# Performance work log

Measured on AMD Instinct MI355X. Metric: run time of the kernel, lower is better.

The kernel has to match this reference:

```python
import jax, jax.numpy as jnp
import numpy as np

N, K, D = 16384, 200, 64  # n_samples, n_components, n_features (8x8 patches)
LOG_2PI = np.float32(np.log(2.0 * np.pi))


def setup_inputs() -> dict:
    rng = np.random.default_rng(0)
    # Build SPD covariances and derive precisions_cholesky exactly like the module:
    # cov_chol = cholesky(cov, lower); prec_chol = solve(cov_chol, I).T
    A = rng.normal(size=(K, D, D))
    cov = A @ A.transpose(0, 2, 1) + D * np.eye(D)  # well-conditioned SPD
    cov_chol = np.linalg.cholesky(cov)  # lower triangular [K,D,D]
    eye = np.broadcast_to(np.eye(D), (K, D, D))
    prec_chol = np.linalg.solve(cov_chol, eye).transpose(0, 2, 1).astype(np.float32)
    means = rng.normal(size=(K, D)).astype(np.float32)
    key = jax.random.key(0)
    x = jax.random.normal(key, (N, D), dtype=jnp.float32)
    return {"x": x, "means": jnp.asarray(means), "prec_chol": jnp.asarray(prec_chol)}


def reference(x, means, prec_chol):
    """Batched GMM log-prob (fused version of estimate_log_prob_torch).

    log_prob[n,k] = -0.5*(D*log(2pi) + ||x_n L_k - mu_k L_k||^2) + log|det L_k|
    where L_k = precisions_cholesky[k].
    """
    n_features = x.shape[1]
    # y[n,k,e] = x @ L_k  -- one batched GEMM instead of K small matmuls
    y = jnp.einsum('nd,kde->nke', x, prec_chol)
    mu_prec = jnp.einsum('kd,kde->ke', means, prec_chol)  # mu_k @ L_k, [K,D]
    log_prob = jnp.sum(jnp.square(y - mu_prec[None, :, :]), axis=-1)  # [N,K]
    # log det of cholesky of precision = sum of log of diagonal entries
    log_det = jnp.sum(jnp.log(jnp.diagonal(prec_chol, axis1=1, axis2=2)), axis=1)  # [K]
    return -0.5 * (n_features * LOG_2PI + log_prob) + log_det[None, :]
```

## Files before the change

### kernel.cpp

```cpp
#include <hip/hip_runtime.h>
#include <hip/hip_bf16.h>
#include <stdint.h>

typedef __bf16 bf16x8 __attribute__((ext_vector_type(8)));
typedef float  f32x4  __attribute__((ext_vector_type(4)));

#define KC 200
#define KB 8
#define CBASE (-58.8120661251f)


__global__ __launch_bounds__(256) void prep_b(const float* __restrict__ prec,
                                              const float* __restrict__ means,
                                              __bf16* __restrict__ Lt,
                                              float* __restrict__ muL,
                                              float* __restrict__ ckh) {
    __shared__ float sP[64][40];
    __shared__ float sM[64];
    const int k = blockIdx.x >> 1, h = blockIdx.x & 1, tid = threadIdx.x;
    const float* pk = prec + (size_t)k * 4096 + h * 32;
    #pragma unroll
    for (int it = 0; it < 2; ++it) {
        int f4 = tid + it * 256;
        int d = f4 >> 3, c = (f4 & 7) * 4;
        float4 v = *(const float4*)(pk + (size_t)d * 64 + c);
        *(float4*)&sP[d][c] = v;
    }
    if (tid < 16) *(float4*)&sM[tid * 4] = ((const float4*)(means + (size_t)k * 64))[tid];
    __syncthreads();
    {
        int e = tid >> 3, d0 = (tid & 7) * 8;
        bf16x8 o;
        #pragma unroll
        for (int i = 0; i < 8; ++i) o[i] = (__bf16)sP[d0 + i][e];
        *(bf16x8*)(Lt + (size_t)k * 4096 + (size_t)(h * 32 + e) * 64 + d0) = o;
    }
    if (tid < 32) {
        int e = tid;
        float m = 0.f;
        #pragma unroll 8
        for (int d = 0; d < 64; ++d) m = fmaf(sM[d], sP[d][e], m);
        muL[k * 64 + h * 32 + e] = m;
        float l = __logf(sP[h * 32 + e][e]);
        #pragma unroll
        for (int mm = 16; mm >= 1; mm >>= 1) l += __shfl_xor(l, mm, 64);
        if (e == 0) ckh[h * KC + k] = l;
    }
}

#define GLL16(gp_, lp_) \
    __builtin_amdgcn_global_load_lds((__attribute__((address_space(1))) const void*)(gp_), \
                                     (__attribute__((address_space(3))) void*)(lp_), 16, 0, 0)

__global__ __launch_bounds__(256, 4) void gmm_main(const float* __restrict__ x,
                                                   const __bf16* __restrict__ Lt,
                                                   const float* __restrict__ muL,
                                                   const float* __restrict__ ckh,
                                                   float* __restrict__ out) {
    __shared__ __align__(16) __bf16 sB[2 * 4096];
    __shared__ __align__(16) float  sOut[256][12];
    __shared__ __align__(16) float  sMu[KB * 64];
    __shared__ float sCk[KB];

    const int tid  = threadIdx.x;
    const int wave = tid >> 6, lane = tid & 63;
    const int li   = lane & 15, q = lane >> 4;
    const int r8   = lane >> 3, s8 = lane & 7;
    const int row0 = blockIdx.x * 256;
    const int rowW = row0 + wave * 64;
    const int k0   = blockIdx.y * KB;
    char* sBc = (char*)sB;

    {
        const __bf16* L0 = Lt + (size_t)k0 * 4096;
        #pragma unroll
        for (int i = 0; i < 2; ++i) {
            int t = wave * 2 + i;
            GLL16(L0 + (size_t)(t * 8 + r8) * 64 + (s8 ^ r8) * 8, sBc + t * 1024);
        }
    }
    if (tid < 128) *(f32x4*)(sMu + tid * 4) = *(const f32x4*)(muL + (size_t)k0 * 64 + tid * 4);
    if (tid < KB)  sCk[tid] = ckh[k0 + tid] + ckh[KC + k0 + tid] + CBASE;

    bf16x8 af[4][2];
    #pragma unroll
    for (int tB = 0; tB < 4; ++tB) {
        const float* xr = x + (size_t)(rowW + 16 * tB + li) * 64 + q * 8;
        #pragma unroll
        for (int ks = 0; ks < 2; ++ks) {
            float4 v0 = *(const float4*)(xr + ks * 32);
            float4 v1 = *(const float4*)(xr + ks * 32 + 4);
            bf16x8 a;
            a[0] = (__bf16)v0.x; a[1] = (__bf16)v0.y; a[2] = (__bf16)v0.z; a[3] = (__bf16)v0.w;
            a[4] = (__bf16)v1.x; a[5] = (__bf16)v1.y; a[6] = (__bf16)v1.z; a[7] = (__bf16)v1.w;
            af[tB][ks] = a;
        }
    }

    #pragma unroll
    for (int kk = 0; kk < KB; ++kk) {
        __syncthreads();
        if (kk + 1 < KB) {
            const __bf16* Ln = Lt + (size_t)(k0 + kk + 1) * 4096;
            char* dst = sBc + ((kk & 1) ^ 1) * 8192;
            #pragma unroll
            for (int i = 0; i < 2; ++i) {
                int t = wave * 2 + i;
                GLL16(Ln + (size_t)(t * 8 + r8) * 64 + (s8 ^ r8) * 8, dst + t * 1024);
            }
        }
        const char* buf = sBc + (kk & 1) * 8192;
        float p[4] = {0.f, 0.f, 0.f, 0.f};

        #pragma unroll
        for (int h = 0; h < 2; ++h) {
            bf16x8 lf[2][2];
            #pragma unroll
            for (int t = 0; t < 2; ++t) {
                int e = 16 * (2 * h + t) + li;
                #pragma unroll
                for (int ks = 0; ks < 2; ++ks)
                    lf[t][ks] = *(const bf16x8*)(buf + e * 128 + (((ks * 4 + q) ^ (li & 7)) << 4));
            }
            f32x4 acc[2][4];
            #pragma unroll
            for (int t = 0; t < 2; ++t) {
                f32x4 mneg = -*(const f32x4*)(sMu + kk * 64 + 16 * (2 * h + t) + 4 * q);
                #pragma unroll
                for (int tB = 0; tB < 4; ++tB) {
                    acc[t][tB] = __builtin_amdgcn_mfma_f32_16x16x32_bf16(
                        lf[t][0], af[tB][0], mneg, 0, 0, 0);
                    acc[t][tB] = __builtin_amdgcn_mfma_f32_16x16x32_bf16(
                        lf[t][1], af[tB][1], acc[t][tB], 0, 0, 0);
                }
            }
            #pragma unroll
            for (int tB = 0; tB < 4; ++tB)
                #pragma unroll
                for (int t = 0; t < 2; ++t)
                    #pragma unroll
                    for (int r = 0; r < 4; ++r)
                        p[tB] = fmaf(acc[t][tB][r], acc[t][tB][r], p[tB]);
        }
        #pragma unroll
        for (int tB = 0; tB < 4; ++tB) {
            p[tB] += __shfl_xor(p[tB], 16, 64);
            p[tB] += __shfl_xor(p[tB], 32, 64);
        }
        float val = (q == 0) ? p[0] : (q == 1) ? p[1] : (q == 2) ? p[2] : p[3];
        sOut[wave * 64 + lane][kk] = fmaf(-0.5f, val, sCk[kk]);
    }
    __syncthreads();

    {
        f32x4 a = *(const f32x4*)&sOut[tid][0];
        f32x4 b = *(const f32x4*)&sOut[tid][4];
        float* op = out + (size_t)(row0 + tid) * KC + k0;
        *(f32x4*)op = a;
        *(f32x4*)(op + 4) = b;
    }
}

extern "C" void kernel_launch(void* const* d_in, const int* in_sizes, int n_in,
                              void* d_out, int out_size, void* d_ws, size_t ws_size,
                              hipStream_t stream) {
    const float* x     = (const float*)d_in[0];
    const float* means = (const float*)d_in[1];
    const float* prec  = (const float*)d_in[2];
    float* out = (float*)d_out;

    __bf16* Lt  = (__bf16*)d_ws;
    float*  muL = (float*)((char*)d_ws + 1638400);
    float*  ckh = (float*)((char*)d_ws + 1689600);

    prep_b<<<400, 256, 0, stream>>>(prec, means, Lt, muL, ckh);
    gmm_main<<<dim3(64, KC / KB), 256, 0, stream>>>(x, Lt, muL, ckh, out);
}
```

Before: 97.41 us.

## Double rows per block to reuse each staged precision tile across more samples

Each block now handles 512 rows instead of 256, with each wave holding 128 rows of x in registers. Every LDS-staged component matrix fragment is therefore reused across twice as many MFMAs, and half as many blocks reload the Lt tiles. The output staging buffer is transposed to a [KB][512] layout to avoid strided LDS writes, and launch bounds drop to 3 waves per SIMD to fit the larger register footprint. The costs are fewer blocks (800), which means less parallelism, and lower occupancy.

```diff
diff --git a/kernel.cpp b/kernel.cpp
--- a/kernel.cpp
+++ b/kernel.cpp
@@ -52,13 +52,13 @@
     __builtin_amdgcn_global_load_lds((__attribute__((address_space(1))) const void*)(gp_), \
                                      (__attribute__((address_space(3))) void*)(lp_), 16, 0, 0)
 
-__global__ __launch_bounds__(256, 4) void gmm_main(const float* __restrict__ x,
+__global__ __launch_bounds__(256, 3) void gmm_main(const float* __restrict__ x,
                                                    const __bf16* __restrict__ Lt,
                                                    const float* __restrict__ muL,
                                                    const float* __restrict__ ckh,
                                                    float* __restrict__ out) {
     __shared__ __align__(16) __bf16 sB[2 * 4096];
-    __shared__ __align__(16) float  sOut[256][12];
+    __shared__ __align__(16) float  sOutT[KB][512];
     __shared__ __align__(16) float  sMu[KB * 64];
     __shared__ float sCk[KB];
 
@@ -66,8 +66,8 @@
     const int wave = tid >> 6, lane = tid & 63;
     const int li   = lane & 15, q = lane >> 4;
     const int r8   = lane >> 3, s8 = lane & 7;
-    const int row0 = blockIdx.x * 256;
-    const int rowW = row0 + wave * 64;
+    const int row0 = blockIdx.x * 512;
+    const int rowW = row0 + wave * 128;
     const int k0   = blockIdx.y * KB;
     char* sBc = (char*)sB;
 
@@ -82,9 +82,9 @@
     if (tid < 128) *(f32x4*)(sMu + tid * 4) = *(const f32x4*)(muL + (size_t)k0 * 64 + tid * 4);
     if (tid < KB)  sCk[tid] = ckh[k0 + tid] + ckh[KC + k0 + tid] + CBASE;
 
-    bf16x8 af[4][2];
+    bf16x8 af[8][2];
     #pragma unroll
-    for (int tB = 0; tB < 4; ++tB) {
+    for (int tB = 0; tB < 8; ++tB) {
         const float* xr = x + (size_t)(rowW + 16 * tB + li) * 64 + q * 8;
         #pragma unroll
         for (int ks = 0; ks < 2; ++ks) {
@@ -110,52 +110,53 @@
             }
         }
         const char* buf = sBc + (kk & 1) * 8192;
-        float p[4] = {0.f, 0.f, 0.f, 0.f};
+        float p[8] = {0.f, 0.f, 0.f, 0.f, 0.f, 0.f, 0.f, 0.f};
 
         #pragma unroll
         for (int h = 0; h < 2; ++h) {
-            bf16x8 lf[2][2];
             #pragma unroll
             for (int t = 0; t < 2; ++t) {
-                int e = 16 * (2 * h + t) + li;
+                const int e = 16 * (2 * h + t) + li;
+                bf16x8 lf0 = *(const bf16x8*)(buf + e * 128 + (((0 * 4 + q) ^ (li & 7)) << 4));
+                bf16x8 lf1 = *(const bf16x8*)(buf + e * 128 + (((1 * 4 + q) ^ (li & 7)) << 4));
+                f32x4 mneg = -*(const f32x4*)(sMu + kk * 64 + 16 * (2 * h + t) + 4 * q);
+                f32x4 acc[8];
                 #pragma unroll
-                for (int ks = 0; ks < 2; ++ks)
-                    lf[t][ks] = *(const bf16x8*)(buf + e * 128 + (((ks * 4 + q) ^ (li & 7)) << 4));
-            }
-            f32x4 acc[2][4];
-            #pragma unroll
-            for (int t = 0; t < 2; ++t) {
-                f32x4 mneg = -*(const f32x4*)(sMu + kk * 64 + 16 * (2 * h + t) + 4 * q);
+                for (int tB = 0; tB < 8; ++tB) {
+                    acc[tB] = __builtin_amdgcn_mfma_f32_16x16x32_bf16(
+                        lf0, af[tB][0], mneg, 0, 0, 0);
+                    acc[tB] = __builtin_amdgcn_mfma_f32_16x16x32_bf16(
+                        lf1, af[tB][1], acc[tB], 0, 0, 0);
+                }
                 #pragma unroll
-                for (int tB = 0; tB < 4; ++tB) {
-                    acc[t][tB] = __builtin_amdgcn_mfma_f32_16x16x32_bf16(
-                        lf[t][0], af[tB][0], mneg, 0, 0, 0);
-                    acc[t][tB] = __builtin_amdgcn_mfma_f32_16x16x32_bf16(
-                        lf[t][1], af[tB][1], acc[t][tB], 0, 0, 0);
-                }
-            }
-            #pragma unroll
-            for (int tB = 0; tB < 4; ++tB)
-                #pragma unroll
-                for (int t = 0; t < 2; ++t)
+                for (int tB = 0; tB < 8; ++tB)
                     #pragma unroll
                     for (int r = 0; r < 4; ++r)
-                        p[tB] = fmaf(acc[t][tB][r], acc[t][tB][r], p[tB]);
+                        p[tB] = fmaf(acc[tB][r], acc[tB][r], p[tB]);
+            }
         }
         #pragma unroll
-        for (int tB = 0; tB < 4; ++tB) {
+        for (int tB = 0; tB < 8; ++tB) {
             p[tB] += __shfl_xor(p[tB], 16, 64);
             p[tB] += __shfl_xor(p[tB], 32, 64);
         }
-        float val = (q == 0) ? p[0] : (q == 1) ? p[1] : (q == 2) ? p[2] : p[3];
-        sOut[wave * 64 + lane][kk] = fmaf(-0.5f, val, sCk[kk]);
+        float v0 = (q == 0) ? p[0] : (q == 1) ? p[1] : (q == 2) ? p[2] : p[3];
+        float v1 = (q == 0) ? p[4] : (q == 1) ? p[5] : (q == 2) ? p[6] : p[7];
+        float c  = sCk[kk];
+        sOutT[kk][wave * 128 + lane]      = fmaf(-0.5f, v0, c);
+        sOutT[kk][wave * 128 + 64 + lane] = fmaf(-0.5f, v1, c);
     }
     __syncthreads();
 
-    {
-        f32x4 a = *(const f32x4*)&sOut[tid][0];
-        f32x4 b = *(const f32x4*)&sOut[tid][4];
-        float* op = out + (size_t)(row0 + tid) * KC + k0;
+    #pragma unroll
+    for (int rr = 0; rr < 2; ++rr) {
+        int r = tid + rr * 256;
+        float vals[KB];
+        #pragma unroll
+        for (int kk = 0; kk < KB; ++kk) vals[kk] = sOutT[kk][r];
+        f32x4 a = {vals[0], vals[1], vals[2], vals[3]};
+        f32x4 b = {vals[4], vals[5], vals[6], vals[7]};
+        float* op = out + (size_t)(row0 + r) * KC + k0;
         *(f32x4*)op = a;
         *(f32x4*)(op + 4) = b;
     }
@@ -174,5 +175,5 @@
     float*  ckh = (float*)((char*)d_ws + 1689600);
 
     prep_b<<<400, 256, 0, stream>>>(prec, means, Lt, muL, ckh);
-    gmm_main<<<dim3(64, KC / KB), 256, 0, stream>>>(x, Lt, muL, ckh, out);
+    gmm_main<<<dim3(32, KC / KB), 256, 0, stream>>>(x, Lt, muL, ckh, out);
 }
```

After: 110.0 us. 13.0% more time.

## Switch GMM main loop to 32x32x16 bf16 MFMA with transposed output staging

Applied to the files above, without the earlier changes.

Replaces the 16x16x32 MFMA tiling with 32x32x16 MFMAs: each wave now computes two 32-row tiles across 32-feature halves with a 16-element accumulator, changing the A/B fragment layouts and the LDS swizzle read pattern. Means are negated once when staged into LDS, squared-norm accumulation uses packed float2 math, and the cross-lane reduction drops to a single shuffle. The output staging buffer is transposed to [KB][256] so per-kk writes are contiguous across lanes. The intent is fewer MFMA issues and fewer shuffle/LDS operations per tile, at the cost of higher accumulator register pressure.

```diff
diff --git a/kernel.cpp b/kernel.cpp
--- a/kernel.cpp
+++ b/kernel.cpp
@@ -4,6 +4,8 @@
 
 typedef __bf16 bf16x8 __attribute__((ext_vector_type(8)));
 typedef float  f32x4  __attribute__((ext_vector_type(4)));
+typedef float  f32x2  __attribute__((ext_vector_type(2)));
+typedef float  f32x16 __attribute__((ext_vector_type(16)));
 
 #define KC 200
 #define KB 8
@@ -58,13 +60,14 @@
                                                    const float* __restrict__ ckh,
                                                    float* __restrict__ out) {
     __shared__ __align__(16) __bf16 sB[2 * 4096];
-    __shared__ __align__(16) float  sOut[256][12];
+    __shared__ __align__(16) float  sOutT[KB][256];
     __shared__ __align__(16) float  sMu[KB * 64];
     __shared__ float sCk[KB];
 
     const int tid  = threadIdx.x;
     const int wave = tid >> 6, lane = tid & 63;
-    const int li   = lane & 15, q = lane >> 4;
+    const int hp   = lane >> 5;
+    const int l31  = lane & 31;
     const int r8   = lane >> 3, s8 = lane & 7;
     const int row0 = blockIdx.x * 256;
     const int rowW = row0 + wave * 64;
@@ -79,21 +82,24 @@
             GLL16(L0 + (size_t)(t * 8 + r8) * 64 + (s8 ^ r8) * 8, sBc + t * 1024);
         }
     }
-    if (tid < 128) *(f32x4*)(sMu + tid * 4) = *(const f32x4*)(muL + (size_t)k0 * 64 + tid * 4);
+    if (tid < 128) {
+        f32x4 v = *(const f32x4*)(muL + (size_t)k0 * 64 + tid * 4);
+        *(f32x4*)(sMu + tid * 4) = -v;
+    }
     if (tid < KB)  sCk[tid] = ckh[k0 + tid] + ckh[KC + k0 + tid] + CBASE;
 
-    bf16x8 af[4][2];
+    bf16x8 af[2][4];
     #pragma unroll
-    for (int tB = 0; tB < 4; ++tB) {
-        const float* xr = x + (size_t)(rowW + 16 * tB + li) * 64 + q * 8;
+    for (int rt = 0; rt < 2; ++rt) {
+        const float* xr = x + (size_t)(rowW + 32 * rt + l31) * 64 + 8 * hp;
         #pragma unroll
-        for (int ks = 0; ks < 2; ++ks) {
-            float4 v0 = *(const float4*)(xr + ks * 32);
-            float4 v1 = *(const float4*)(xr + ks * 32 + 4);
+        for (int ki = 0; ki < 4; ++ki) {
+            float4 v0 = *(const float4*)(xr + 16 * ki);
+            float4 v1 = *(const float4*)(xr + 16 * ki + 4);
             bf16x8 a;
             a[0] = (__bf16)v0.x; a[1] = (__bf16)v0.y; a[2] = (__bf16)v0.z; a[3] = (__bf16)v0.w;
             a[4] = (__bf16)v1.x; a[5] = (__bf16)v1.y; a[6] = (__bf16)v1.z; a[7] = (__bf16)v1.w;
-            af[tB][ks] = a;
+            af[rt][ki] = a;
         }
     }
 
@@ -110,51 +116,56 @@
             }
         }
         const char* buf = sBc + (kk & 1) * 8192;
-        float p[4] = {0.f, 0.f, 0.f, 0.f};
+        f32x2 p2[2] = {(f32x2){0.f, 0.f}, (f32x2){0.f, 0.f}};
 
         #pragma unroll
-        for (int h = 0; h < 2; ++h) {
-            bf16x8 lf[2][2];
+        for (int et = 0; et < 2; ++et) {
+            const int e = et * 32 + l31;
+            bf16x8 lf[4];
             #pragma unroll
-            for (int t = 0; t < 2; ++t) {
-                int e = 16 * (2 * h + t) + li;
+            for (int ki = 0; ki < 4; ++ki) {
+                int slot = (2 * ki + hp) ^ (lane & 7);
+                lf[ki] = *(const bf16x8*)(buf + e * 128 + (slot << 4));
+            }
+            f32x16 c0;
+            #pragma unroll
+            for (int rq = 0; rq < 4; ++rq) {
+                f32x4 m = *(const f32x4*)(sMu + kk * 64 + et * 32 + 8 * rq + 4 * hp);
+                c0[4 * rq + 0] = m[0]; c0[4 * rq + 1] = m[1];
+                c0[4 * rq + 2] = m[2]; c0[4 * rq + 3] = m[3];
+            }
+            f32x16 acc[2];
+            #pragma unroll
+            for (int rt = 0; rt < 2; ++rt) {
+                acc[rt] = c0;
                 #pragma unroll
-                for (int ks = 0; ks < 2; ++ks)
-                    lf[t][ks] = *(const bf16x8*)(buf + e * 128 + (((ks * 4 + q) ^ (li & 7)) << 4));
-            }
-            f32x4 acc[2][4];
-            #pragma unroll
-            for (int t = 0; t < 2; ++t) {
-                f32x4 mneg = -*(const f32x4*)(sMu + kk * 64 + 16 * (2 * h + t) + 4 * q);
-                #pragma unroll
-                for (int tB = 0; tB < 4; ++tB) {
-                    acc[t][tB] = __builtin_amdgcn_mfma_f32_16x16x32_bf16(
-                        lf[t][0], af[tB][0], mneg, 0, 0, 0);
-                    acc[t][tB] = __builtin_amdgcn_mfma_f32_16x16x32_bf16(
-                        lf[t][1], af[tB][1], acc[t][tB], 0, 0, 0);
-                }
+                for (int ki = 0; ki < 4; ++ki)
+                    acc[rt] = __builtin_amdgcn_mfma_f32_32x32x16_bf16(
+                        lf[ki], af[rt][ki], acc[rt], 0, 0, 0);
             }
             #pragma unroll
-            for (int tB = 0; tB < 4; ++tB)
+            for (int rt = 0; rt < 2; ++rt)
                 #pragma unroll
-                for (int t = 0; t < 2; ++t)
-                    #pragma unroll
-                    for (int r = 0; r < 4; ++r)
-                        p[tB] = fmaf(acc[t][tB][r], acc[t][tB][r], p[tB]);
+                for (int i = 0; i < 8; ++i) {
+                    f32x2 pa = {acc[rt][2 * i], acc[rt][2 * i + 1]};
+                    p2[rt] += pa * pa;
+                }
         }
-        #pragma unroll
-        for (int tB = 0; tB < 4; ++tB) {
-            p[tB] += __shfl_xor(p[tB], 16, 64);
-            p[tB] += __shfl_xor(p[tB], 32, 64);
-        }
-        float val = (q == 0) ? p[0] : (q == 1) ? p[1] : (q == 2) ? p[2] : p[3];
-        sOut[wave * 64 + lane][kk] = fmaf(-0.5f, val, sCk[kk]);
+        float pr0 = p2[0][0] + p2[0][1];
+        float pr1 = p2[1][0] + p2[1][1];
+        pr0 += __shfl_xor(pr0, 32, 64);
+        pr1 += __shfl_xor(pr1, 32, 64);
+        float val = hp ? pr1 : pr0;
+        sOutT[kk][wave * 64 + lane] = fmaf(-0.5f, val, sCk[kk]);
     }
     __syncthreads();
 
     {
-        f32x4 a = *(const f32x4*)&sOut[tid][0];
-        f32x4 b = *(const f32x4*)&sOut[tid][4];
+        float vals[KB];
+        #pragma unroll
+        for (int kk = 0; kk < KB; ++kk) vals[kk] = sOutT[kk][tid];
+        f32x4 a = {vals[0], vals[1], vals[2], vals[3]};
+        f32x4 b = {vals[4], vals[5], vals[6], vals[7]};
         float* op = out + (size_t)(row0 + tid) * KC + k0;
         *(f32x4*)op = a;
         *(f32x4*)(op + 4) = b;
```

New measurement: 98.18 us. About the same (+0.8%).
